# Kernel optimization log

Hardware: AMD Instinct MI355X
Metric: run time of the kernel (lower is better)

The kernel has to match this reference:

```python
import jax, jax.numpy as jnp
import numpy as np

N_SEQ, SEQ_LEN, HIDDEN, BATCH = 2048, 128, 128, 64


def setup_inputs() -> dict:
    key = jax.random.key(0)
    ks = jax.random.split(key, 6)
    s_ih = 1.0 / np.sqrt(SEQ_LEN)
    s_hh = 1.0 / np.sqrt(HIDDEN)
    s_fc = 1.0 / np.sqrt(N_SEQ * HIDDEN)
    return {
        "x": jax.random.normal(ks[0], (BATCH, N_SEQ, SEQ_LEN), dtype=jnp.float32),
        "h0": jnp.zeros((BATCH, HIDDEN), dtype=jnp.float32),
        "c0": jnp.zeros((BATCH, HIDDEN), dtype=jnp.float32),
        # LSTM weights, PyTorch gate order (i, f, g, o) packed on last axis
        "W_ih": jax.random.uniform(ks[1], (SEQ_LEN, 4 * HIDDEN), jnp.float32, -s_ih, s_ih),
        "W_hh": jax.random.uniform(ks[2], (HIDDEN, 4 * HIDDEN), jnp.float32, -s_hh, s_hh),
        "b": jax.random.uniform(ks[3], (4 * HIDDEN,), jnp.float32, -s_ih, s_ih),
        "fc_w": jax.random.uniform(ks[4], (2, N_SEQ * HIDDEN), jnp.float32, -s_fc, s_fc),
        "fc_b": jax.random.uniform(ks[5], (2,), jnp.float32, -s_fc, s_fc),
    }


def _lstm(x_tmajor, h0, c0, W_ih, W_hh, b):
    # x_tmajor: [T, B, D]. Precompute input projection in one big matmul.
    pre = jnp.einsum("tbd,dg->tbg", x_tmajor, W_ih) + b  # [T, B, 4H]
    H = h0.shape[-1]

    def step(carry, pre_t):
        h, c = carry
        gates = pre_t + h @ W_hh  # [B, 4H]
        i = jax.nn.sigmoid(gates[:, 0 * H:1 * H])
        f = jax.nn.sigmoid(gates[:, 1 * H:2 * H])
        g = jnp.tanh(gates[:, 2 * H:3 * H])
        o = jax.nn.sigmoid(gates[:, 3 * H:4 * H])
        c_new = f * c + i * g
        h_new = o * jnp.tanh(c_new)
        return (h_new, c_new), h_new

    (_, _), hs = jax.lax.scan(step, (h0, c0), pre)
    return hs  # [T, B, H]


def reference(x, h0, c0, W_ih, W_hh, b, fc_w, fc_b):
    xt = jnp.transpose(x, (1, 0, 2))              # [T, B, D]
    hs = _lstm(xt, h0, c0, W_ih, W_hh, b)          # [T, B, H]
    hb = jnp.transpose(hs, (1, 0, 2))              # [B, T, H]
    flat = hb.reshape(hb.shape[0], -1)             # [B, T*H]
    return flat @ fc_w.T + fc_b                    # [B, 2]
```

## Files before the change

### kernel.cpp

```cpp
#include <hip/hip_runtime.h>

#define T_SEQ 2048
#define NBATCH 64
#define DIM 128
#define HID 128
#define G4 512
#define GRP 16
#define TT 8

typedef _Float16 h2v   __attribute__((ext_vector_type(2)));
typedef _Float16 f16x8 __attribute__((ext_vector_type(8)));
typedef float    f32x4 __attribute__((ext_vector_type(4)));

__device__ __forceinline__ unsigned pack2(float lo, float hi) {
    h2v v; v.x = (_Float16)lo; v.y = (_Float16)hi;
    return __builtin_bit_cast(unsigned, v);
}
__device__ __forceinline__ float dot2(unsigned a, unsigned b, float c) {
#if __has_builtin(__builtin_amdgcn_fdot2)
    return __builtin_amdgcn_fdot2(__builtin_bit_cast(h2v, a),
                                  __builtin_bit_cast(h2v, b), c, false);
#else
    h2v av = __builtin_bit_cast(h2v, a), bv = __builtin_bit_cast(h2v, b);
    c = fmaf((float)av.x, (float)bv.x, c);
    return fmaf((float)av.y, (float)bv.y, c);
#endif
}
__device__ __forceinline__ float rcp_(float x) { return __builtin_amdgcn_rcpf(x); }
__device__ __forceinline__ float sigmoidf_(float x) {
    return rcp_(1.0f + __expf(-x));
}
__device__ __forceinline__ float tanhf_(float x) {
    return fmaf(2.0f, rcp_(1.0f + __expf(-2.0f * x)), -1.0f);
}
template <int CTRL>
__device__ __forceinline__ float qmov(float v) {
    int r = __builtin_amdgcn_mov_dpp(__builtin_bit_cast(int, v), CTRL, 0xF, 0xF, true);
    return __builtin_bit_cast(float, r);
}
#define QP_XOR1 0xB1
#define QP_XOR2 0x4E
#define QP_B0   0x00
#define QP_B1   0x55
#define QP_B2   0xAA
#define QP_B3   0xFF

__device__ __forceinline__ void barrier_lgkm() {
    asm volatile("s_waitcnt lgkmcnt(0)\n\ts_barrier" ::: "memory");
    __builtin_amdgcn_sched_barrier(0);
}

__global__ __launch_bounds__(256) void prep(
    const float* __restrict__ x, _Float16* __restrict__ x16)
{
    const size_t gtid   = (size_t)blockIdx.x * blockDim.x + threadIdx.x;
    const size_t stride = (size_t)gridDim.x * blockDim.x;
    const size_t n_x2 = (size_t)NBATCH * T_SEQ * DIM / 2;
    for (size_t i = gtid; i < n_x2; i += stride) {
        float2 v = reinterpret_cast<const float2*>(x)[i];
        h2v p; p.x = (_Float16)v.x; p.y = (_Float16)v.y;
        reinterpret_cast<h2v*>(x16)[i] = p;
    }
}

__global__ __launch_bounds__(512, 2) void pre_mfma(
    const _Float16* __restrict__ x16,
    const float* __restrict__ Wih,
    const float* __restrict__ bias,
    _Float16* __restrict__ pre,
    int t0)
{
    const int tid = threadIdx.x;
    const int w   = tid >> 6;
    const int l   = tid & 63;
    const int col = l & 15;
    const int hi  = l >> 4;
    const int bg  = blockIdx.x & 3;
    const int lt0 = (blockIdx.x >> 2) * TT;
    const int batch = bg * 16 + col;

    f16x8 aX[4][4];
    f32x4 bv[4];
    #pragma unroll
    for (int j = 0; j < 4; ++j) {
        const int chr  = 16 * (4 * w + j) + col;
        const int wcol = (chr & 3) * HID + (chr >> 2);
        #pragma unroll
        for (int ks = 0; ks < 4; ++ks) {
            f16x8 a;
            #pragma unroll
            for (int i = 0; i < 8; ++i) {
                int k = ks * 32 + hi * 8 + i;
                a[i] = (_Float16)Wih[(size_t)k * G4 + wcol];
            }
            aX[j][ks] = a;
        }
        #pragma unroll
        for (int r = 0; r < 4; ++r) {
            const int ch = 16 * (4 * w + j) + 4 * hi + r;
            bv[j][r] = bias[(ch & 3) * HID + (ch >> 2)];
        }
    }

    const _Float16* xb_base = x16 + (size_t)batch * T_SEQ * DIM + hi * 8;

    for (int tt = 0; tt < TT; ++tt) {
        const int lt = lt0 + tt;
        const int t  = t0 + lt;
        f16x8 xf[4];
        #pragma unroll
        for (int ks = 0; ks < 4; ++ks)
            xf[ks] = *reinterpret_cast<const f16x8*>(
                xb_base + (size_t)t * DIM + ks * 32);
        #pragma unroll
        for (int j = 0; j < 4; ++j) {
            f32x4 acc = bv[j];
            #pragma unroll
            for (int ks = 0; ks < 4; ++ks)
                acc = __builtin_amdgcn_mfma_f32_16x16x32_f16(aX[j][ks], xf[ks], acc, 0, 0, 0);
            uint2 o;
            o.x = pack2(acc[0], acc[1]);
            o.y = pack2(acc[2], acc[3]);
            *reinterpret_cast<uint2*>(
                pre + ((size_t)lt * NBATCH + batch) * G4 + 16 * (4 * w + j) + 4 * hi) = o;
        }
    }
}

__global__ __launch_bounds__(512, 1) void lstm_scan(
    const _Float16* __restrict__ pre,
    const float* __restrict__ Whh,
    const float* __restrict__ h0,
    const float* __restrict__ c0,
    const float* __restrict__ fcw,
    const float* __restrict__ fcb,
    float* __restrict__ state,
    float* __restrict__ out,
    int t0, int tc)
{
    __shared__ __align__(16) _Float16 h_sh[2][HID];
    __shared__ float red[2][HID];

    const int tid = threadIdx.x;
    const int j = tid >> 2;
    const int q = tid & 3;
    const int b = blockIdx.x;
    const bool q1 = (q & 1) != 0;
    const bool q2 = (q & 2) != 0;
    const bool isg = (q == 2);

    float* st_h  = state;
    float* st_c  = state + NBATCH * HID;
    float* st_f0 = state + 2 * NBATCH * HID;
    float* st_f1 = state + 3 * NBATCH * HID;

    unsigned wpk[4][16];
    #pragma unroll
    for (int g = 0; g < 4; ++g)
        #pragma unroll
        for (int i = 0; i < 16; ++i) {
            int k0 = q * 32 + 2 * i;
            wpk[g][i] = pack2(Whh[(size_t)k0 * G4 + g * HID + j],
                              Whh[(size_t)(k0 + 1) * G4 + g * HID + j]);
        }

    float c, facc = 0.f, hj;
    if (t0 == 0) {
        hj = h0[b * HID + j]; c = c0[b * HID + j];
    } else {
        hj = st_h[b * HID + j];
        c  = st_c[b * HID + j];
        if (q == 2) facc = st_f0[b * HID + j];
        if (q == 3) facc = st_f1[b * HID + j];
    }
    if (q == 0) h_sh[0][j] = (_Float16)hj;

    const float* fp = fcw + ((q == 3) ? (size_t)T_SEQ * HID : 0) + j;
    const size_t pstep = (size_t)NBATCH * G4;
    const _Float16* pb = pre + (size_t)b * G4 + tid;

    unsigned short prA[GRP], prB[GRP];
    float fwA[GRP], fwB[GRP];
    #pragma unroll
    for (int s = 0; s < GRP; ++s)
        prA[s] = __builtin_bit_cast(unsigned short, pb[(size_t)s * pstep]);
    if (q >= 2) {
        #pragma unroll
        for (int s = 0; s < GRP; ++s)
            fwA[s] = fp[(size_t)(t0 + s) * HID];
    }

    __syncthreads();

#define LOADG(PR, FW, TGN)                                                   \
    {                                                                        \
        const int tgl = (TGN);                                               \
        _Pragma("unroll")                                                    \
        for (int s = 0; s < GRP; ++s)                                        \
            PR[s] = __builtin_bit_cast(unsigned short,                       \
                        pb[(size_t)(tgl + s) * pstep]);                      \
        if (q >= 2) {                                                        \
            _Pragma("unroll")                                                \
            for (int s = 0; s < GRP; ++s)                                    \
                FW[s] = fp[(size_t)(t0 + tgl + s) * HID];                    \
        }                                                                    \
    }

#define STEP16(PR, FW)                                                       \
    _Pragma("unroll")                                                        \
    for (int s = 0; s < GRP; ++s) {                                          \
        const int cur = s & 1;                                               \
        const uint4* hp = reinterpret_cast<const uint4*>(&h_sh[cur][q * 32]);\
        float pv = (float)__builtin_bit_cast(_Float16, PR[s]);               \
        float a0 = (q == 0) ? pv : 0.f;                                      \
        float a1 = (q == 1) ? pv : 0.f;                                      \
        float a2 = (q == 2) ? pv : 0.f;                                      \
        float a3 = (q == 3) ? pv : 0.f;                                      \
        _Pragma("unroll")                                                    \
        for (int m = 0; m < 4; ++m) {                                        \
            uint4 hv = hp[m];                                                \
            a0 = dot2(hv.x, wpk[0][4 * m + 0], a0);                          \
            a1 = dot2(hv.x, wpk[1][4 * m + 0], a1);                          \
            a2 = dot2(hv.x, wpk[2][4 * m + 0], a2);                          \
            a3 = dot2(hv.x, wpk[3][4 * m + 0], a3);                          \
            a0 = dot2(hv.y, wpk[0][4 * m + 1], a0);                          \
            a1 = dot2(hv.y, wpk[1][4 * m + 1], a1);                          \
            a2 = dot2(hv.y, wpk[2][4 * m + 1], a2);                          \
            a3 = dot2(hv.y, wpk[3][4 * m + 1], a3);                          \
            a0 = dot2(hv.z, wpk[0][4 * m + 2], a0);                          \
            a1 = dot2(hv.z, wpk[1][4 * m + 2], a1);                          \
            a2 = dot2(hv.z, wpk[2][4 * m + 2], a2);                          \
            a3 = dot2(hv.z, wpk[3][4 * m + 2], a3);                          \
            a0 = dot2(hv.w, wpk[0][4 * m + 3], a0);                          \
            a1 = dot2(hv.w, wpk[1][4 * m + 3], a1);                          \
            a2 = dot2(hv.w, wpk[2][4 * m + 3], a2);                          \
            a3 = dot2(hv.w, wpk[3][4 * m + 3], a3);                          \
        }                                                                    \
        float t01  = q1 ? a1 : a0;                                           \
        float t01o = q1 ? a0 : a1;                                           \
        t01 += qmov<QP_XOR1>(t01o);                                          \
        float t23  = q1 ? a3 : a2;                                           \
        float t23o = q1 ? a2 : a3;                                           \
        t23 += qmov<QP_XOR1>(t23o);                                          \
        float tq  = q2 ? t23 : t01;                                          \
        float tqo = q2 ? t01 : t23;                                          \
        tq += qmov<QP_XOR2>(tqo);                                            \
        float e   = __expf(isg ? -2.0f * tq : -tq);                          \
        float v   = rcp_(1.0f + e);                                          \
        float act = isg ? fmaf(2.0f, v, -1.0f) : v;                          \
        float gi = qmov<QP_B0>(act);                                         \
        float gf = qmov<QP_B1>(act);                                         \
        float gg = qmov<QP_B2>(act);                                         \
        float go = qmov<QP_B3>(act);                                         \
        c = fmaf(gf, c, gi * gg);                                            \
        float hn = go * tanhf_(c);                                           \
        hj = hn;                                                             \
        if (q == 0) h_sh[cur ^ 1][j] = (_Float16)hn;                         \
        if (q >= 2) facc = fmaf(hn, FW[s], facc);                            \
        barrier_lgkm();                                                      \
    }

    for (int tg = 0; tg < tc; tg += 2 * GRP) {
        LOADG(prB, fwB, tg + GRP);
        STEP16(prA, fwA);
        const int tga = (tg + 2 * GRP < tc) ? tg + 2 * GRP : tg;
        LOADG(prA, fwA, tga);
        STEP16(prB, fwB);
    }
#undef LOADG
#undef STEP16

    if (t0 + tc >= T_SEQ) {
        if (q == 2) red[0][j] = facc;
        if (q == 3) red[1][j] = facc;
        __syncthreads();
        if (tid < 128) {
            int o = tid >> 6;
            int l = tid & 63;
            float v = red[o][l] + red[o][l + 64];
            v += __shfl_xor(v, 32); v += __shfl_xor(v, 16);
            v += __shfl_xor(v, 8);  v += __shfl_xor(v, 4);
            v += __shfl_xor(v, 2);  v += __shfl_xor(v, 1);
            if (l == 0) out[b * 2 + o] = v + fcb[o];
        }
    } else {
        if (q == 0) { st_h[b * HID + j] = hj; st_c[b * HID + j] = c; }
        if (q == 2) st_f0[b * HID + j] = facc;
        if (q == 3) st_f1[b * HID + j] = facc;
    }
}

extern "C" void kernel_launch(void* const* d_in, const int* in_sizes, int n_in,
                              void* d_out, int out_size, void* d_ws, size_t ws_size,
                              hipStream_t stream) {
    const float* x    = (const float*)d_in[0];
    const float* h0   = (const float*)d_in[1];
    const float* c0   = (const float*)d_in[2];
    const float* Wih  = (const float*)d_in[3];
    const float* Whh  = (const float*)d_in[4];
    const float* bias = (const float*)d_in[5];
    const float* fcw  = (const float*)d_in[6];
    const float* fcb  = (const float*)d_in[7];
    float* out = (float*)d_out;

    char* wsb = (char*)d_ws;
    _Float16* x16 = (_Float16*)wsb;
    float* state  = (float*)(wsb + (size_t)NBATCH * T_SEQ * DIM * 2);
    const size_t state_floats = (size_t)4 * NBATCH * HID;
    _Float16* pre = (_Float16*)(state + state_floats);

    const size_t head = (size_t)NBATCH * T_SEQ * DIM * 2 + state_floats * 4;
    const size_t per_t_bytes = (size_t)NBATCH * G4 * sizeof(_Float16);
    size_t avail = (ws_size > head) ? ws_size - head : 0;
    int Tc = (int)(avail / per_t_bytes);
    Tc &= ~(2 * GRP - 1);
    if (Tc < 2 * GRP) Tc = 2 * GRP;
    if (Tc > T_SEQ) Tc = T_SEQ;

    prep<<<512, 256, 0, stream>>>(x, x16);
    for (int t0 = 0; t0 < T_SEQ; t0 += Tc) {
        int tc = (t0 + Tc <= T_SEQ) ? Tc : (T_SEQ - t0);
        pre_mfma<<<(tc / TT) * 4, 512, 0, stream>>>(x16, Wih, bias, pre, t0);
        lstm_scan<<<64, 512, 0, stream>>>(pre, Whh, h0, c0, fcw, fcb,
                                          state, out, t0, tc);
    }
}
```

Measured before the change: 1.200 ms.

## Fold exp2 scaling into weights, defer FC head to separate kernel via h trace

Pre-scales the input and recurrent weights and the bias by -log2e (or -2log2e for the g gate), so each step's activation needs only exp2 and rcp, and sigmoid/tanh share one path. The tanh on g is rewritten algebraically inside the c update. The per-step FC accumulation and its fcw loads are removed from the serial scan. Instead h is written as fp16 to a trace buffer and reduced afterwards by a new parallel fc_head kernel. This shortens the latency-critical recurrent step, at the cost of extra workspace, a trace write each step and an fp16-rounded h in the FC dot product.

New measurement: 1.162 ms. 3.2% less time.

```diff
diff --git a/kernel.cpp b/kernel.cpp
--- a/kernel.cpp
+++ b/kernel.cpp
@@ -7,6 +7,7 @@
 #define G4 512
 #define GRP 16
 #define TT 8
+#define LOG2E 1.44269504088896f
 
 typedef _Float16 h2v   __attribute__((ext_vector_type(2)));
 typedef _Float16 f16x8 __attribute__((ext_vector_type(8)));
@@ -26,13 +27,8 @@
     return fmaf((float)av.y, (float)bv.y, c);
 #endif
 }
-__device__ __forceinline__ float rcp_(float x) { return __builtin_amdgcn_rcpf(x); }
-__device__ __forceinline__ float sigmoidf_(float x) {
-    return rcp_(1.0f + __expf(-x));
-}
-__device__ __forceinline__ float tanhf_(float x) {
-    return fmaf(2.0f, rcp_(1.0f + __expf(-2.0f * x)), -1.0f);
-}
+__device__ __forceinline__ float rcp_(float x)  { return __builtin_amdgcn_rcpf(x); }
+__device__ __forceinline__ float exp2_(float x) { return __builtin_amdgcn_exp2f(x); }
 template <int CTRL>
 __device__ __forceinline__ float qmov(float v) {
     int r = __builtin_amdgcn_mov_dpp(__builtin_bit_cast(int, v), CTRL, 0xF, 0xF, true);
@@ -85,20 +81,22 @@
     for (int j = 0; j < 4; ++j) {
         const int chr  = 16 * (4 * w + j) + col;
         const int wcol = (chr & 3) * HID + (chr >> 2);
+        const float sc = ((chr & 3) == 2) ? -2.0f * LOG2E : -LOG2E;
         #pragma unroll
         for (int ks = 0; ks < 4; ++ks) {
             f16x8 a;
             #pragma unroll
             for (int i = 0; i < 8; ++i) {
                 int k = ks * 32 + hi * 8 + i;
-                a[i] = (_Float16)Wih[(size_t)k * G4 + wcol];
+                a[i] = (_Float16)(Wih[(size_t)k * G4 + wcol] * sc);
             }
             aX[j][ks] = a;
         }
         #pragma unroll
         for (int r = 0; r < 4; ++r) {
             const int ch = 16 * (4 * w + j) + 4 * hi + r;
-            bv[j][r] = bias[(ch & 3) * HID + (ch >> 2)];
+            const float scr = ((ch & 3) == 2) ? -2.0f * LOG2E : -LOG2E;
+            bv[j][r] = bias[(ch & 3) * HID + (ch >> 2)] * scr;
         }
     }
 
@@ -132,14 +130,11 @@
     const float* __restrict__ Whh,
     const float* __restrict__ h0,
     const float* __restrict__ c0,
-    const float* __restrict__ fcw,
-    const float* __restrict__ fcb,
     float* __restrict__ state,
-    float* __restrict__ out,
+    _Float16* __restrict__ trace,
     int t0, int tc)
 {
     __shared__ __align__(16) _Float16 h_sh[2][HID];
-    __shared__ float red[2][HID];
 
     const int tid = threadIdx.x;
     const int j = tid >> 2;
@@ -147,75 +142,57 @@
     const int b = blockIdx.x;
     const bool q1 = (q & 1) != 0;
     const bool q2 = (q & 2) != 0;
-    const bool isg = (q == 2);
-
-    float* st_h  = state;
-    float* st_c  = state + NBATCH * HID;
-    float* st_f0 = state + 2 * NBATCH * HID;
-    float* st_f1 = state + 3 * NBATCH * HID;
+
+    float* st_h = state;
+    float* st_c = state + NBATCH * HID;
 
     unsigned wpk[4][16];
     #pragma unroll
-    for (int g = 0; g < 4; ++g)
+    for (int g = 0; g < 4; ++g) {
+        const float sc = (g == 2) ? -2.0f * LOG2E : -LOG2E;
         #pragma unroll
         for (int i = 0; i < 16; ++i) {
             int k0 = q * 32 + 2 * i;
-            wpk[g][i] = pack2(Whh[(size_t)k0 * G4 + g * HID + j],
-                              Whh[(size_t)(k0 + 1) * G4 + g * HID + j]);
-        }
-
-    float c, facc = 0.f, hj;
+            wpk[g][i] = pack2(Whh[(size_t)k0 * G4 + g * HID + j] * sc,
+                              Whh[(size_t)(k0 + 1) * G4 + g * HID + j] * sc);
+        }
+    }
+
+    float c, hj;
     if (t0 == 0) {
         hj = h0[b * HID + j]; c = c0[b * HID + j];
     } else {
         hj = st_h[b * HID + j];
         c  = st_c[b * HID + j];
-        if (q == 2) facc = st_f0[b * HID + j];
-        if (q == 3) facc = st_f1[b * HID + j];
     }
     if (q == 0) h_sh[0][j] = (_Float16)hj;
 
-    const float* fp = fcw + ((q == 3) ? (size_t)T_SEQ * HID : 0) + j;
     const size_t pstep = (size_t)NBATCH * G4;
     const _Float16* pb = pre + (size_t)b * G4 + tid;
+    _Float16* tb = trace + ((size_t)b * T_SEQ + t0) * HID + j;
 
     unsigned short prA[GRP], prB[GRP];
-    float fwA[GRP], fwB[GRP];
     #pragma unroll
     for (int s = 0; s < GRP; ++s)
         prA[s] = __builtin_bit_cast(unsigned short, pb[(size_t)s * pstep]);
-    if (q >= 2) {
-        #pragma unroll
-        for (int s = 0; s < GRP; ++s)
-            fwA[s] = fp[(size_t)(t0 + s) * HID];
-    }
 
     __syncthreads();
 
-#define LOADG(PR, FW, TGN)                                                   \
+#define LOADG(PR, TGN)                                                       \
     {                                                                        \
         const int tgl = (TGN);                                               \
         _Pragma("unroll")                                                    \
         for (int s = 0; s < GRP; ++s)                                        \
             PR[s] = __builtin_bit_cast(unsigned short,                       \
                         pb[(size_t)(tgl + s) * pstep]);                      \
-        if (q >= 2) {                                                        \
-            _Pragma("unroll")                                                \
-            for (int s = 0; s < GRP; ++s)                                    \
-                FW[s] = fp[(size_t)(t0 + tgl + s) * HID];                    \
-        }                                                                    \
-    }
-
-#define STEP16(PR, FW)                                                       \
+    }
+
+#define STEP16(PR, TG)                                                       \
     _Pragma("unroll")                                                        \
     for (int s = 0; s < GRP; ++s) {                                          \
         const int cur = s & 1;                                               \
         const uint4* hp = reinterpret_cast<const uint4*>(&h_sh[cur][q * 32]);\
-        float pv = (float)__builtin_bit_cast(_Float16, PR[s]);               \
-        float a0 = (q == 0) ? pv : 0.f;                                      \
-        float a1 = (q == 1) ? pv : 0.f;                                      \
-        float a2 = (q == 2) ? pv : 0.f;                                      \
-        float a3 = (q == 3) ? pv : 0.f;                                      \
+        float a0 = 0.f, a1 = 0.f, a2 = 0.f, a3 = 0.f;                        \
         _Pragma("unroll")                                                    \
         for (int m = 0; m < 4; ++m) {                                        \
             uint4 hv = hp[m];                                                \
@@ -245,48 +222,81 @@
         float tq  = q2 ? t23 : t01;                                          \
         float tqo = q2 ? t01 : t23;                                          \
         tq += qmov<QP_XOR2>(tqo);                                            \
-        float e   = __expf(isg ? -2.0f * tq : -tq);                          \
-        float v   = rcp_(1.0f + e);                                          \
-        float act = isg ? fmaf(2.0f, v, -1.0f) : v;                          \
-        float gi = qmov<QP_B0>(act);                                         \
-        float gf = qmov<QP_B1>(act);                                         \
-        float gg = qmov<QP_B2>(act);                                         \
-        float go = qmov<QP_B3>(act);                                         \
-        c = fmaf(gf, c, gi * gg);                                            \
-        float hn = go * tanhf_(c);                                           \
+        tq += (float)__builtin_bit_cast(_Float16, PR[s]);                    \
+        float v = rcp_(1.0f + exp2_(tq));                                    \
+        float gi = qmov<QP_B0>(v);                                           \
+        float gf = qmov<QP_B1>(v);                                           \
+        float vg = qmov<QP_B2>(v);                                           \
+        float go = qmov<QP_B3>(v);                                           \
+        c = fmaf(gf, c, fmaf(gi + gi, vg, -gi));                             \
+        float vc = rcp_(1.0f + exp2_(-2.0f * LOG2E * c));                    \
+        float hn = fmaf(go + go, vc, -go);                                   \
         hj = hn;                                                             \
-        if (q == 0) h_sh[cur ^ 1][j] = (_Float16)hn;                         \
-        if (q >= 2) facc = fmaf(hn, FW[s], facc);                            \
+        _Float16 h16 = (_Float16)hn;                                         \
+        if (q == 0) {                                                        \
+            h_sh[cur ^ 1][j] = h16;                                          \
+            tb[(size_t)((TG) + s) * HID] = h16;                              \
+        }                                                                    \
         barrier_lgkm();                                                      \
     }
 
     for (int tg = 0; tg < tc; tg += 2 * GRP) {
-        LOADG(prB, fwB, tg + GRP);
-        STEP16(prA, fwA);
+        LOADG(prB, tg + GRP);
+        STEP16(prA, tg);
         const int tga = (tg + 2 * GRP < tc) ? tg + 2 * GRP : tg;
-        LOADG(prA, fwA, tga);
-        STEP16(prB, fwB);
+        LOADG(prA, tga);
+        STEP16(prB, tg + GRP);
     }
 #undef LOADG
 #undef STEP16
 
-    if (t0 + tc >= T_SEQ) {
-        if (q == 2) red[0][j] = facc;
-        if (q == 3) red[1][j] = facc;
-        __syncthreads();
-        if (tid < 128) {
-            int o = tid >> 6;
-            int l = tid & 63;
-            float v = red[o][l] + red[o][l + 64];
-            v += __shfl_xor(v, 32); v += __shfl_xor(v, 16);
-            v += __shfl_xor(v, 8);  v += __shfl_xor(v, 4);
-            v += __shfl_xor(v, 2);  v += __shfl_xor(v, 1);
-            if (l == 0) out[b * 2 + o] = v + fcb[o];
-        }
-    } else {
+    if (t0 + tc < T_SEQ) {
         if (q == 0) { st_h[b * HID + j] = hj; st_c[b * HID + j] = c; }
-        if (q == 2) st_f0[b * HID + j] = facc;
-        if (q == 3) st_f1[b * HID + j] = facc;
+    }
+}
+
+__global__ __launch_bounds__(256) void fc_head(
+    const _Float16* __restrict__ trace,
+    const float* __restrict__ fcw,
+    const float* __restrict__ fcb,
+    float* __restrict__ out)
+{
+    __shared__ float red[4][2];
+    const int b = blockIdx.x, tid = threadIdx.x;
+    const _Float16* tbase = trace + (size_t)b * (T_SEQ * HID);
+    const float* w0 = fcw;
+    const float* w1 = fcw + (size_t)T_SEQ * HID;
+
+    float s0 = 0.f, s1 = 0.f;
+    for (int i = tid * 8; i < T_SEQ * HID; i += 256 * 8) {
+        uint4 tv = *reinterpret_cast<const uint4*>(tbase + i);
+        float wa0[8], wa1[8];
+        *reinterpret_cast<float4*>(&wa0[0]) = *reinterpret_cast<const float4*>(w0 + i);
+        *reinterpret_cast<float4*>(&wa0[4]) = *reinterpret_cast<const float4*>(w0 + i + 4);
+        *reinterpret_cast<float4*>(&wa1[0]) = *reinterpret_cast<const float4*>(w1 + i);
+        *reinterpret_cast<float4*>(&wa1[4]) = *reinterpret_cast<const float4*>(w1 + i + 4);
+        const unsigned* tw = reinterpret_cast<const unsigned*>(&tv);
+        #pragma unroll
+        for (int e = 0; e < 4; ++e) {
+            h2v hh = __builtin_bit_cast(h2v, tw[e]);
+            float hx = (float)hh.x, hy = (float)hh.y;
+            s0 = fmaf(hx, wa0[2 * e], s0);
+            s0 = fmaf(hy, wa0[2 * e + 1], s0);
+            s1 = fmaf(hx, wa1[2 * e], s1);
+            s1 = fmaf(hy, wa1[2 * e + 1], s1);
+        }
+    }
+    #pragma unroll
+    for (int d = 32; d >= 1; d >>= 1) {
+        s0 += __shfl_xor(s0, d);
+        s1 += __shfl_xor(s1, d);
+    }
+    const int w = tid >> 6;
+    if ((tid & 63) == 0) { red[w][0] = s0; red[w][1] = s1; }
+    __syncthreads();
+    if (tid < 2) {
+        float v = red[0][tid] + red[1][tid] + red[2][tid] + red[3][tid];
+        out[b * 2 + tid] = v + fcb[tid];
     }
 }
 
@@ -304,12 +314,13 @@
     float* out = (float*)d_out;
 
     char* wsb = (char*)d_ws;
-    _Float16* x16 = (_Float16*)wsb;
-    float* state  = (float*)(wsb + (size_t)NBATCH * T_SEQ * DIM * 2);
-    const size_t state_floats = (size_t)4 * NBATCH * HID;
+    _Float16* x16   = (_Float16*)wsb;
+    _Float16* trace = (_Float16*)(wsb + (size_t)NBATCH * T_SEQ * DIM * 2);
+    float* state    = (float*)(wsb + 2 * (size_t)NBATCH * T_SEQ * DIM * 2);
+    const size_t state_floats = (size_t)2 * NBATCH * HID;
     _Float16* pre = (_Float16*)(state + state_floats);
 
-    const size_t head = (size_t)NBATCH * T_SEQ * DIM * 2 + state_floats * 4;
+    const size_t head = 2 * (size_t)NBATCH * T_SEQ * DIM * 2 + state_floats * 4;
     const size_t per_t_bytes = (size_t)NBATCH * G4 * sizeof(_Float16);
     size_t avail = (ws_size > head) ? ws_size - head : 0;
     int Tc = (int)(avail / per_t_bytes);
@@ -321,7 +332,7 @@
     for (int t0 = 0; t0 < T_SEQ; t0 += Tc) {
         int tc = (t0 + Tc <= T_SEQ) ? Tc : (T_SEQ - t0);
         pre_mfma<<<(tc / TT) * 4, 512, 0, stream>>>(x16, Wih, bias, pre, t0);
-        lstm_scan<<<64, 512, 0, stream>>>(pre, Whh, h0, c0, fcw, fcb,
-                                          state, out, t0, tc);
-    }
-}
+        lstm_scan<<<64, 512, 0, stream>>>(pre, Whh, h0, c0, state, trace, t0, tc);
+    }
+    fc_head<<<64, 256, 0, stream>>>(trace, fcw, fcb, out);
+}
```
